# Performance work log

Measured on AMD Instinct MI355X. Metric: run time of the kernel, lower is better.

The kernel has to match this reference:

```python
import jax, jax.numpy as jnp
import numpy as np

EMBED_DIM = 1024
NUM_HEADS = 16
HEAD_DIM = EMBED_DIM // NUM_HEADS  # 64


def setup_inputs() -> dict:
    key = jax.random.key(0)
    k1, k2, k3 = jax.random.split(key, 3)
    B, N = 2, 2048
    x = jax.random.normal(k1, (B, N, EMBED_DIM), dtype=jnp.float32)
    # torch nn.Linear(E, 3E): y = x @ W.T + b; we store W already transposed as [E, 3E]
    W_qkv = jax.random.normal(k2, (EMBED_DIM, 3 * EMBED_DIM), dtype=jnp.float32) * (EMBED_DIM ** -0.5)
    b_qkv = jax.random.normal(k3, (3 * EMBED_DIM,), dtype=jnp.float32) * 0.02
    return {"x": x, "W_qkv": W_qkv, "b_qkv": b_qkv}


def reference(x, W_qkv, b_qkv):
    B, N, E = x.shape
    H, e = NUM_HEADS, HEAD_DIM
    y = x @ W_qkv + b_qkv                      # [B, N, 3E]
    # einops: 'b n (e k) -> b n e k' (k=3) then 'b n (e H) k -> b H n e k'
    # => flat index into 3E is (e_idx*H + h)*3 + qkv_idx
    y = y.reshape(B, N, e, H, 3)
    y = jnp.transpose(y, (0, 3, 1, 2, 4))      # [B, H, N, e, 3]
    q, k, v = y[..., 0], y[..., 1], y[..., 2]  # each [B, H, N, e]
    scale = 1.0 / jnp.sqrt(jnp.asarray(H, dtype=x.dtype))  # note: sqrt(num_heads), per source
    scores = jnp.einsum('bhne,bhme->bhnm', q, k) * scale   # [B, H, N, N]
    wei = jax.nn.softmax(scores, axis=-1)
    out = jnp.einsum('bhnm,bhme->bhne', wei, v)            # [B, H, N, e]
    # 'b H n e -> b n (H e)'; dropout is identity in eval mode
    out = jnp.transpose(out, (0, 2, 1, 3)).reshape(B, N, H * e)
    return out
```

## Files before the change

kernel.cpp:

```cpp
#include <hip/hip_runtime.h>
#include <hip/hip_bf16.h>
#include <math.h>

#define EDIM 1024
#define N3E  3072
#define NSEQ 2048
#define NB   2
#define NH   16
#define HD   64
#define MTOT (NB*NSEQ)

typedef __attribute__((ext_vector_type(8))) short bf16x8;
typedef __attribute__((ext_vector_type(4))) float f32x4;

#define SCALE2 0.360673760222241f

__device__ __forceinline__ short f2bf(float f) {
    union { float f; unsigned u; } v; v.f = f;
    unsigned r = v.u + 0x7FFFu + ((v.u >> 16) & 1u);
    return (short)(r >> 16);
}

__device__ __forceinline__ unsigned cvtpk(float lo, float hi) {
    unsigned r;
    asm("v_cvt_pk_bf16_f32 %0, %1, %2" : "=v"(r) : "v"(lo), "v"(hi));
    return r;
}

__device__ __forceinline__ void gload16(const void* g, void* l) {
    __builtin_amdgcn_global_load_lds(
        (const __attribute__((address_space(1))) unsigned int*)g,
        (__attribute__((address_space(3))) unsigned int*)l, 16, 0, 0);
}

__global__ __launch_bounds__(256) void k_convert_x(const float* __restrict__ x,
                                                   short* __restrict__ xb, int n4) {
    int i = blockIdx.x * blockDim.x + threadIdx.x;
    int stride = gridDim.x * blockDim.x;
    for (; i < n4; i += stride) {
        float4 v = ((const float4*)x)[i];
        ushort4 o;
        o.x = (unsigned short)f2bf(v.x);
        o.y = (unsigned short)f2bf(v.y);
        o.z = (unsigned short)f2bf(v.z);
        o.w = (unsigned short)f2bf(v.w);
        ((ushort4*)xb)[i] = o;
    }
}

__global__ __launch_bounds__(256) void k_transpose_w(const float* __restrict__ w,
                                                     short* __restrict__ wt) {
    __shared__ float T[96][68];
    int k0 = blockIdx.x * 64;
    int c0 = blockIdx.y * 96;
    int t = threadIdx.x;
    {
        int kr = t >> 2;
        int cb = (t & 3) * 24;
        const float* src = w + (size_t)(k0 + kr) * N3E + c0 + cb;
        #pragma unroll
        for (int i = 0; i < 24; i += 4) {
            float4 v = *(const float4*)(src + i);
            T[cb + i + 0][kr] = v.x;
            T[cb + i + 1][kr] = v.y;
            T[cb + i + 2][kr] = v.z;
            T[cb + i + 3][kr] = v.w;
        }
    }
    __syncthreads();
    int kk = (t & 7) * 8;
    #pragma unroll
    for (int p = 0; p < 3; ++p) {
        int cc = p * 32 + (t >> 3);
        int ca = c0 + cc;
        int e = ca / 48, h = (ca % 48) / 3, q = ca % 3;
        int cp = q * 1024 + h * 64 + e;
        bf16x8 o;
        #pragma unroll
        for (int j = 0; j < 8; ++j) o[j] = f2bf(T[cc][kk + j]);
        *(bf16x8*)(wt + (size_t)cp * EDIM + k0 + kk) = o;
    }
}

__global__ void k_perm_bias(const float* __restrict__ b, float* __restrict__ bp) {
    int c = blockIdx.x * 256 + threadIdx.x;
    if (c >= N3E) return;
    int e = c / 48, h = (c % 48) / 3, q = c % 3;
    bp[q * 1024 + h * 64 + e] = b[c];
}

__global__ __launch_bounds__(256) void k_qkv_gemm(const short* __restrict__ xb,
        const short* __restrict__ wt, const float* __restrict__ bp,
        short* __restrict__ qkv) {
    __shared__ short Al[128][32];
    __shared__ short Bl[128][32];
    int t = threadIdx.x, lane = t & 63, wv = t >> 6;
    int g = lane >> 4, r = lane & 15;
    int wr = wv >> 1, wc = wv & 1;
    int m0 = blockIdx.x * 128, n0 = blockIdx.y * 128;
    int srow = wv * 32 + (lane >> 2);
    int scol = (lane & 3) * 8;
    const short* ga0 = xb + (size_t)(m0 + srow) * EDIM + scol;
    const short* ga1 = ga0 + (size_t)16 * EDIM;
    const short* gb0 = wt + (size_t)(n0 + srow) * EDIM + scol;
    const short* gb1 = gb0 + (size_t)16 * EDIM;
    char* la0 = (char*)(&Al[0][0]) + wv * 2048;
    char* lb0 = (char*)(&Bl[0][0]) + wv * 2048;
    f32x4 acc[4][4] = {};
    for (int k0 = 0; k0 < EDIM; k0 += 32) {
        gload16(ga0 + k0, la0);
        gload16(ga1 + k0, la0 + 1024);
        gload16(gb0 + k0, lb0);
        gload16(gb1 + k0, lb0 + 1024);
        __syncthreads();
        bf16x8 af[4], bfr[4];
        #pragma unroll
        for (int mt = 0; mt < 4; ++mt)
            af[mt] = *(const bf16x8*)(&Al[wr*64 + mt*16 + r][g*8]);
        #pragma unroll
        for (int nt = 0; nt < 4; ++nt)
            bfr[nt] = *(const bf16x8*)(&Bl[wc*64 + nt*16 + r][g*8]);
        #pragma unroll
        for (int mt = 0; mt < 4; ++mt)
            #pragma unroll
            for (int nt = 0; nt < 4; ++nt)
                acc[mt][nt] = __builtin_amdgcn_mfma_f32_16x16x32_bf16(
                                  af[mt], bfr[nt], acc[mt][nt], 0, 0, 0);
        __syncthreads();
    }
    #pragma unroll
    for (int nt = 0; nt < 4; ++nt) {
        int cp = n0 + wc*64 + nt*16 + r;
        float bias = bp[cp];
        int q = cp >> 10, h = (cp >> 6) & 15, e = cp & 63;
        #pragma unroll
        for (int mt = 0; mt < 4; ++mt) {
            #pragma unroll
            for (int rg = 0; rg < 4; ++rg) {
                int m = m0 + wr*64 + mt*16 + g*4 + rg;
                int bb = m >> 11, n = m & 2047;
                qkv[((((size_t)q*NB + bb)*NH + h)*NSEQ + n)*HD + e] =
                    f2bf(acc[mt][nt][rg] + bias);
            }
        }
    }
}

__global__ __launch_bounds__(256) void k_attn(const short* __restrict__ qkv,
                                              float* __restrict__ out) {
    __shared__ short Kl[64][72];
    __shared__ short Vt[64][72];
    __shared__ short Pl[4][2][16][64];
    int t = threadIdx.x, lane = t & 63, wv = t >> 6;
    int g = lane >> 4, r = lane & 15;
    int qb = blockIdx.x, h = blockIdx.y, b = blockIdx.z;
    const size_t HS = (size_t)NSEQ * HD;
    const short* Qp = qkv + ((size_t)(0*NB + b)*NH + h) * HS;
    const short* Kp = qkv + ((size_t)(1*NB + b)*NH + h) * HS;
    const short* Vp = qkv + ((size_t)(2*NB + b)*NH + h) * HS;
    int q0 = qb * 128 + wv * 32;
    bf16x8 qf00 = *(const bf16x8*)(Qp + (size_t)(q0 + r)*HD + g*8);
    bf16x8 qf01 = *(const bf16x8*)(Qp + (size_t)(q0 + r)*HD + 32 + g*8);
    bf16x8 qf10 = *(const bf16x8*)(Qp + (size_t)(q0 + 16 + r)*HD + g*8);
    bf16x8 qf11 = *(const bf16x8*)(Qp + (size_t)(q0 + 16 + r)*HD + 32 + g*8);
    f32x4 o0[4] = {}, o1[4] = {};
    float m0r = -3.0e38f, m1r = -3.0e38f, l0r = 0.f, l1r = 0.f;
    int skv = t >> 2, sd = (t & 3) * 16;
    int vkv = (t >> 4) * 4, vd = (t & 15) * 4;
    int rx = (r & 7) << 4;
    char* prow0 = (char*)(&Pl[wv][0][0][0]) + r * 128;
    char* prow1 = prow0 + 2048;
    bf16x8 kk0, kk1; ushort4 vv0, vv1, vv2, vv3;
    const short* Kst = Kp + (size_t)skv * HD + sd;
    const short* Vst = Vp + (size_t)vkv * HD + vd;
    kk0 = *(const bf16x8*)(Kst);
    kk1 = *(const bf16x8*)(Kst + 8);
    vv0 = *(const ushort4*)(Vst);
    vv1 = *(const ushort4*)(Vst + HD);
    vv2 = *(const ushort4*)(Vst + 2*HD);
    vv3 = *(const ushort4*)(Vst + 3*HD);
    {
        *(bf16x8*)(&Kl[skv][sd]) = kk0;
        *(bf16x8*)(&Kl[skv][sd + 8]) = kk1;
        #pragma unroll
        for (int i = 0; i < 4; ++i) {
            unsigned lo = (unsigned)((const unsigned short*)&vv0)[i]
                        | ((unsigned)((const unsigned short*)&vv1)[i] << 16);
            unsigned hi = (unsigned)((const unsigned short*)&vv2)[i]
                        | ((unsigned)((const unsigned short*)&vv3)[i] << 16);
            uint2 wrd; wrd.x = lo; wrd.y = hi;
            *(uint2*)(&Vt[vd + i][vkv]) = wrd;
        }
    }
    for (int kt = 0; kt < NSEQ; kt += 64) {
        __syncthreads();
        bool more = (kt + 64) < NSEQ;
        if (more) {
            kk0 = *(const bf16x8*)(Kst + (size_t)(kt + 64) * HD);
            kk1 = *(const bf16x8*)(Kst + (size_t)(kt + 64) * HD + 8);
            vv0 = *(const ushort4*)(Vst + (size_t)(kt + 64) * HD);
            vv1 = *(const ushort4*)(Vst + (size_t)(kt + 65) * HD);
            vv2 = *(const ushort4*)(Vst + (size_t)(kt + 66) * HD);
            vv3 = *(const ushort4*)(Vst + (size_t)(kt + 67) * HD);
        }
        f32x4 s0[4], s1[4];
        #pragma unroll
        for (int jt = 0; jt < 4; ++jt) {
            bf16x8 kf0 = *(const bf16x8*)(&Kl[jt*16 + r][g*8]);
            bf16x8 kf1 = *(const bf16x8*)(&Kl[jt*16 + r][32 + g*8]);
            f32x4 z = {};
            s0[jt] = __builtin_amdgcn_mfma_f32_16x16x32_bf16(kf0, qf00, z, 0,0,0);
            s0[jt] = __builtin_amdgcn_mfma_f32_16x16x32_bf16(kf1, qf01, s0[jt], 0,0,0);
            s1[jt] = __builtin_amdgcn_mfma_f32_16x16x32_bf16(kf0, qf10, z, 0,0,0);
            s1[jt] = __builtin_amdgcn_mfma_f32_16x16x32_bf16(kf1, qf11, s1[jt], 0,0,0);
        }
        bf16x8 vf[4][2];
        #pragma unroll
        for (int dt = 0; dt < 4; ++dt) {
            vf[dt][0] = *(const bf16x8*)(&Vt[dt*16 + r][g*8]);
            vf[dt][1] = *(const bf16x8*)(&Vt[dt*16 + r][32 + g*8]);
        }
        {
            float mx = s0[0][0];
            #pragma unroll
            for (int jt = 0; jt < 4; ++jt)
                #pragma unroll
                for (int rg = 0; rg < 4; ++rg) mx = fmaxf(mx, s0[jt][rg]);
            mx = fmaxf(mx, __shfl_xor(mx, 16));
            mx = fmaxf(mx, __shfl_xor(mx, 32));
            float mnew = fmaxf(m0r, mx);
            float a = exp2f(SCALE2 * (m0r - mnew));
            m0r = mnew;
            float cm = SCALE2 * mnew;
            float ps = 0.f;
            #pragma unroll
            for (int jt = 0; jt < 4; ++jt) {
                float p0 = exp2f(fmaf(SCALE2, s0[jt][0], -cm));
                float p1 = exp2f(fmaf(SCALE2, s0[jt][1], -cm));
                float p2 = exp2f(fmaf(SCALE2, s0[jt][2], -cm));
                float p3 = exp2f(fmaf(SCALE2, s0[jt][3], -cm));
                ps += (p0 + p1) + (p2 + p3);
                uint2 wrd; wrd.x = cvtpk(p0, p1); wrd.y = cvtpk(p2, p3);
                *(uint2*)(prow0 + ((32*jt + 8*g) ^ rx)) = wrd;
            }
            ps += __shfl_xor(ps, 16);
            ps += __shfl_xor(ps, 32);
            l0r = l0r * a + ps;
            #pragma unroll
            for (int dt = 0; dt < 4; ++dt) o0[dt] *= a;
            bf16x8 pb0 = *(const bf16x8*)(prow0 + ((16*g) ^ rx));
            bf16x8 pb1 = *(const bf16x8*)(prow0 + ((64 + 16*g) ^ rx));
            #pragma unroll
            for (int dt = 0; dt < 4; ++dt) {
                o0[dt] = __builtin_amdgcn_mfma_f32_16x16x32_bf16(vf[dt][0], pb0, o0[dt], 0,0,0);
                o0[dt] = __builtin_amdgcn_mfma_f32_16x16x32_bf16(vf[dt][1], pb1, o0[dt], 0,0,0);
            }
        }
        {
            float mx = s1[0][0];
            #pragma unroll
            for (int jt = 0; jt < 4; ++jt)
                #pragma unroll
                for (int rg = 0; rg < 4; ++rg) mx = fmaxf(mx, s1[jt][rg]);
            mx = fmaxf(mx, __shfl_xor(mx, 16));
            mx = fmaxf(mx, __shfl_xor(mx, 32));
            float mnew = fmaxf(m1r, mx);
            float a = exp2f(SCALE2 * (m1r - mnew));
            m1r = mnew;
            float cm = SCALE2 * mnew;
            float ps = 0.f;
            #pragma unroll
            for (int jt = 0; jt < 4; ++jt) {
                float p0 = exp2f(fmaf(SCALE2, s1[jt][0], -cm));
                float p1 = exp2f(fmaf(SCALE2, s1[jt][1], -cm));
                float p2 = exp2f(fmaf(SCALE2, s1[jt][2], -cm));
                float p3 = exp2f(fmaf(SCALE2, s1[jt][3], -cm));
                ps += (p0 + p1) + (p2 + p3);
                uint2 wrd; wrd.x = cvtpk(p0, p1); wrd.y = cvtpk(p2, p3);
                *(uint2*)(prow1 + ((32*jt + 8*g) ^ rx)) = wrd;
            }
            ps += __shfl_xor(ps, 16);
            ps += __shfl_xor(ps, 32);
            l1r = l1r * a + ps;
            #pragma unroll
            for (int dt = 0; dt < 4; ++dt) o1[dt] *= a;
            bf16x8 pb0 = *(const bf16x8*)(prow1 + ((16*g) ^ rx));
            bf16x8 pb1 = *(const bf16x8*)(prow1 + ((64 + 16*g) ^ rx));
            #pragma unroll
            for (int dt = 0; dt < 4; ++dt) {
                o1[dt] = __builtin_amdgcn_mfma_f32_16x16x32_bf16(vf[dt][0], pb0, o1[dt], 0,0,0);
                o1[dt] = __builtin_amdgcn_mfma_f32_16x16x32_bf16(vf[dt][1], pb1, o1[dt], 0,0,0);
            }
        }
        __syncthreads();
        if (more) {
            *(bf16x8*)(&Kl[skv][sd]) = kk0;
            *(bf16x8*)(&Kl[skv][sd + 8]) = kk1;
            #pragma unroll
            for (int i = 0; i < 4; ++i) {
                unsigned lo = (unsigned)((const unsigned short*)&vv0)[i]
                            | ((unsigned)((const unsigned short*)&vv1)[i] << 16);
                unsigned hi = (unsigned)((const unsigned short*)&vv2)[i]
                            | ((unsigned)((const unsigned short*)&vv3)[i] << 16);
                uint2 wrd; wrd.x = lo; wrd.y = hi;
                *(uint2*)(&Vt[vd + i][vkv]) = wrd;
            }
        }
    }
    float inv0 = 1.0f / l0r, inv1 = 1.0f / l1r;
    #pragma unroll
    for (int dt = 0; dt < 4; ++dt) {
        float4 v0, v1;
        v0.x = o0[dt][0]*inv0; v0.y = o0[dt][1]*inv0;
        v0.z = o0[dt][2]*inv0; v0.w = o0[dt][3]*inv0;
        v1.x = o1[dt][0]*inv1; v1.y = o1[dt][1]*inv1;
        v1.z = o1[dt][2]*inv1; v1.w = o1[dt][3]*inv1;
        *(float4*)(out + (size_t)(b*NSEQ + q0 + r)*EDIM + h*HD + dt*16 + g*4) = v0;
        *(float4*)(out + (size_t)(b*NSEQ + q0 + 16 + r)*EDIM + h*HD + dt*16 + g*4) = v1;
    }
}

extern "C" void kernel_launch(void* const* d_in, const int* in_sizes, int n_in,
                              void* d_out, int out_size, void* d_ws, size_t ws_size,
                              hipStream_t stream) {
    const float* x  = (const float*)d_in[0];
    const float* w  = (const float*)d_in[1];
    const float* bq = (const float*)d_in[2];
    float* outp = (float*)d_out;
    char* ws = (char*)d_ws;
    short* Xb  = (short*)(ws);
    short* Wt  = (short*)(ws + 8388608);
    float* Bp  = (float*)(ws + 8388608 + 6291456);
    short* QKV = (short*)(ws + 8388608 + 6291456 + 16384);
    k_convert_x<<<dim3(2048), dim3(256), 0, stream>>>(x, Xb, (MTOT*EDIM)/4);
    k_transpose_w<<<dim3(16, 32), dim3(256), 0, stream>>>(w, Wt);
    k_perm_bias<<<dim3(12), dim3(256), 0, stream>>>(bq, Bp);
    k_qkv_gemm<<<dim3(32, 24), dim3(256), 0, stream>>>(Xb, Wt, Bp, QKV);
    k_attn<<<dim3(16, 16, 2), dim3(256), 0, stream>>>(QKV, outp);
}
```

Measured before the change: 220.4 us.

## Double-buffer QKV GEMM with swizzle; shrink attention tile and add lazy rescale

The QKV GEMM now double-buffers its LDS tiles so the next K-slice loads while MFMAs run on the current one. It also remaps block indices with a swizzle to improve cache locality. The attention kernel moves from 32 to 16 queries per wave, which doubles the grid, and shrinks the LDS padding. It also skips the online-softmax rescale when the running max grows by less than a threshold. The smaller query tile raises occupancy and parallelism but doubles the K/V traffic per query. The 68-element padding may give misaligned 16-byte LDS accesses.

```diff
diff --git a/kernel.cpp b/kernel.cpp
--- a/kernel.cpp
+++ b/kernel.cpp
@@ -14,6 +14,7 @@
 typedef __attribute__((ext_vector_type(4))) float f32x4;
 
 #define SCALE2 0.360673760222241f
+#define DTHR   16.0f
 
 __device__ __forceinline__ short f2bf(float f) {
     union { float f; unsigned u; } v; v.f = f;
@@ -92,34 +93,45 @@
 __global__ __launch_bounds__(256) void k_qkv_gemm(const short* __restrict__ xb,
         const short* __restrict__ wt, const float* __restrict__ bp,
         short* __restrict__ qkv) {
-    __shared__ short Al[128][32];
-    __shared__ short Bl[128][32];
+    __shared__ short Al[2][128][32];
+    __shared__ short Bl[2][128][32];
     int t = threadIdx.x, lane = t & 63, wv = t >> 6;
     int g = lane >> 4, r = lane & 15;
     int wr = wv >> 1, wc = wv & 1;
-    int m0 = blockIdx.x * 128, n0 = blockIdx.y * 128;
+    int flat = blockIdx.y * 32 + blockIdx.x;
+    int sw = (flat & 7) * 96 + (flat >> 3);
+    int m0 = (sw & 31) * 128, n0 = (sw >> 5) * 128;
     int srow = wv * 32 + (lane >> 2);
     int scol = (lane & 3) * 8;
     const short* ga0 = xb + (size_t)(m0 + srow) * EDIM + scol;
     const short* ga1 = ga0 + (size_t)16 * EDIM;
     const short* gb0 = wt + (size_t)(n0 + srow) * EDIM + scol;
     const short* gb1 = gb0 + (size_t)16 * EDIM;
-    char* la0 = (char*)(&Al[0][0]) + wv * 2048;
-    char* lb0 = (char*)(&Bl[0][0]) + wv * 2048;
+    char* laA = (char*)(&Al[0][0][0]) + wv * 2048;
+    char* laB = (char*)(&Bl[0][0][0]) + wv * 2048;
     f32x4 acc[4][4] = {};
-    for (int k0 = 0; k0 < EDIM; k0 += 32) {
-        gload16(ga0 + k0, la0);
-        gload16(ga1 + k0, la0 + 1024);
-        gload16(gb0 + k0, lb0);
-        gload16(gb1 + k0, lb0 + 1024);
-        __syncthreads();
+    gload16(ga0, laA);
+    gload16(ga1, laA + 1024);
+    gload16(gb0, laB);
+    gload16(gb1, laB + 1024);
+    __syncthreads();
+    for (int step = 0; step < 32; ++step) {
+        if (step < 31) {
+            int nk = (step + 1) * 32;
+            int bo = ((step + 1) & 1) * 8192;
+            gload16(ga0 + nk, laA + bo);
+            gload16(ga1 + nk, laA + bo + 1024);
+            gload16(gb0 + nk, laB + bo);
+            gload16(gb1 + nk, laB + bo + 1024);
+        }
+        int cb = step & 1;
         bf16x8 af[4], bfr[4];
         #pragma unroll
         for (int mt = 0; mt < 4; ++mt)
-            af[mt] = *(const bf16x8*)(&Al[wr*64 + mt*16 + r][g*8]);
+            af[mt] = *(const bf16x8*)(&Al[cb][wr*64 + mt*16 + r][g*8]);
         #pragma unroll
         for (int nt = 0; nt < 4; ++nt)
-            bfr[nt] = *(const bf16x8*)(&Bl[wc*64 + nt*16 + r][g*8]);
+            bfr[nt] = *(const bf16x8*)(&Bl[cb][wc*64 + nt*16 + r][g*8]);
         #pragma unroll
         for (int mt = 0; mt < 4; ++mt)
             #pragma unroll
@@ -148,9 +160,9 @@
 
 __global__ __launch_bounds__(256) void k_attn(const short* __restrict__ qkv,
                                               float* __restrict__ out) {
-    __shared__ short Kl[64][72];
-    __shared__ short Vt[64][72];
-    __shared__ short Pl[4][2][16][64];
+    __shared__ short Kl[64][68];
+    __shared__ short Vt[64][68];
+    __shared__ short Pl[4][16][64];
     int t = threadIdx.x, lane = t & 63, wv = t >> 6;
     int g = lane >> 4, r = lane & 15;
     int qb = blockIdx.x, h = blockIdx.y, b = blockIdx.z;
@@ -158,18 +170,15 @@
     const short* Qp = qkv + ((size_t)(0*NB + b)*NH + h) * HS;
     const short* Kp = qkv + ((size_t)(1*NB + b)*NH + h) * HS;
     const short* Vp = qkv + ((size_t)(2*NB + b)*NH + h) * HS;
-    int q0 = qb * 128 + wv * 32;
-    bf16x8 qf00 = *(const bf16x8*)(Qp + (size_t)(q0 + r)*HD + g*8);
-    bf16x8 qf01 = *(const bf16x8*)(Qp + (size_t)(q0 + r)*HD + 32 + g*8);
-    bf16x8 qf10 = *(const bf16x8*)(Qp + (size_t)(q0 + 16 + r)*HD + g*8);
-    bf16x8 qf11 = *(const bf16x8*)(Qp + (size_t)(q0 + 16 + r)*HD + 32 + g*8);
-    f32x4 o0[4] = {}, o1[4] = {};
-    float m0r = -3.0e38f, m1r = -3.0e38f, l0r = 0.f, l1r = 0.f;
+    int q0 = qb * 64 + wv * 16;
+    bf16x8 qf0 = *(const bf16x8*)(Qp + (size_t)(q0 + r)*HD + g*8);
+    bf16x8 qf1 = *(const bf16x8*)(Qp + (size_t)(q0 + r)*HD + 32 + g*8);
+    f32x4 o[4] = {};
+    float mr = -3.0e38f, lr = 0.f;
     int skv = t >> 2, sd = (t & 3) * 16;
     int vkv = (t >> 4) * 4, vd = (t & 15) * 4;
     int rx = (r & 7) << 4;
-    char* prow0 = (char*)(&Pl[wv][0][0][0]) + r * 128;
-    char* prow1 = prow0 + 2048;
+    char* prow = (char*)(&Pl[wv][0][0]) + r * 128;
     bf16x8 kk0, kk1; ushort4 vv0, vv1, vv2, vv3;
     const short* Kst = Kp + (size_t)skv * HD + sd;
     const short* Vst = Vp + (size_t)vkv * HD + vd;
@@ -203,16 +212,14 @@
             vv2 = *(const ushort4*)(Vst + (size_t)(kt + 66) * HD);
             vv3 = *(const ushort4*)(Vst + (size_t)(kt + 67) * HD);
         }
-        f32x4 s0[4], s1[4];
+        f32x4 s[4];
         #pragma unroll
         for (int jt = 0; jt < 4; ++jt) {
             bf16x8 kf0 = *(const bf16x8*)(&Kl[jt*16 + r][g*8]);
             bf16x8 kf1 = *(const bf16x8*)(&Kl[jt*16 + r][32 + g*8]);
             f32x4 z = {};
-            s0[jt] = __builtin_amdgcn_mfma_f32_16x16x32_bf16(kf0, qf00, z, 0,0,0);
-            s0[jt] = __builtin_amdgcn_mfma_f32_16x16x32_bf16(kf1, qf01, s0[jt], 0,0,0);
-            s1[jt] = __builtin_amdgcn_mfma_f32_16x16x32_bf16(kf0, qf10, z, 0,0,0);
-            s1[jt] = __builtin_amdgcn_mfma_f32_16x16x32_bf16(kf1, qf11, s1[jt], 0,0,0);
+            s[jt] = __builtin_amdgcn_mfma_f32_16x16x32_bf16(kf0, qf0, z, 0,0,0);
+            s[jt] = __builtin_amdgcn_mfma_f32_16x16x32_bf16(kf1, qf1, s[jt], 0,0,0);
         }
         bf16x8 vf[4][2];
         #pragma unroll
@@ -220,77 +227,41 @@
             vf[dt][0] = *(const bf16x8*)(&Vt[dt*16 + r][g*8]);
             vf[dt][1] = *(const bf16x8*)(&Vt[dt*16 + r][32 + g*8]);
         }
-        {
-            float mx = s0[0][0];
+        float mx = fmaxf(fmaxf(fmaxf(s[0][0], s[0][1]), fmaxf(s[0][2], s[0][3])),
+                         fmaxf(fmaxf(s[1][0], s[1][1]), fmaxf(s[1][2], s[1][3])));
+        mx = fmaxf(mx, fmaxf(fmaxf(fmaxf(s[2][0], s[2][1]), fmaxf(s[2][2], s[2][3])),
+                             fmaxf(fmaxf(s[3][0], s[3][1]), fmaxf(s[3][2], s[3][3]))));
+        mx = fmaxf(mx, __shfl_xor(mx, 16));
+        mx = fmaxf(mx, __shfl_xor(mx, 32));
+        if (!__all(mx <= mr + DTHR)) {
+            float mnew = fmaxf(mr, mx);
+            float a = exp2f(SCALE2 * (mr - mnew));
+            mr = mnew;
+            lr *= a;
             #pragma unroll
-            for (int jt = 0; jt < 4; ++jt)
-                #pragma unroll
-                for (int rg = 0; rg < 4; ++rg) mx = fmaxf(mx, s0[jt][rg]);
-            mx = fmaxf(mx, __shfl_xor(mx, 16));
-            mx = fmaxf(mx, __shfl_xor(mx, 32));
-            float mnew = fmaxf(m0r, mx);
-            float a = exp2f(SCALE2 * (m0r - mnew));
-            m0r = mnew;
-            float cm = SCALE2 * mnew;
-            float ps = 0.f;
-            #pragma unroll
-            for (int jt = 0; jt < 4; ++jt) {
-                float p0 = exp2f(fmaf(SCALE2, s0[jt][0], -cm));
-                float p1 = exp2f(fmaf(SCALE2, s0[jt][1], -cm));
-                float p2 = exp2f(fmaf(SCALE2, s0[jt][2], -cm));
-                float p3 = exp2f(fmaf(SCALE2, s0[jt][3], -cm));
-                ps += (p0 + p1) + (p2 + p3);
-                uint2 wrd; wrd.x = cvtpk(p0, p1); wrd.y = cvtpk(p2, p3);
-                *(uint2*)(prow0 + ((32*jt + 8*g) ^ rx)) = wrd;
-            }
-            ps += __shfl_xor(ps, 16);
-            ps += __shfl_xor(ps, 32);
-            l0r = l0r * a + ps;
-            #pragma unroll
-            for (int dt = 0; dt < 4; ++dt) o0[dt] *= a;
-            bf16x8 pb0 = *(const bf16x8*)(prow0 + ((16*g) ^ rx));
-            bf16x8 pb1 = *(const bf16x8*)(prow0 + ((64 + 16*g) ^ rx));
-            #pragma unroll
-            for (int dt = 0; dt < 4; ++dt) {
-                o0[dt] = __builtin_amdgcn_mfma_f32_16x16x32_bf16(vf[dt][0], pb0, o0[dt], 0,0,0);
-                o0[dt] = __builtin_amdgcn_mfma_f32_16x16x32_bf16(vf[dt][1], pb1, o0[dt], 0,0,0);
-            }
-        }
-        {
-            float mx = s1[0][0];
-            #pragma unroll
-            for (int jt = 0; jt < 4; ++jt)
-                #pragma unroll
-                for (int rg = 0; rg < 4; ++rg) mx = fmaxf(mx, s1[jt][rg]);
-            mx = fmaxf(mx, __shfl_xor(mx, 16));
-            mx = fmaxf(mx, __shfl_xor(mx, 32));
-            float mnew = fmaxf(m1r, mx);
-            float a = exp2f(SCALE2 * (m1r - mnew));
-            m1r = mnew;
-            float cm = SCALE2 * mnew;
-            float ps = 0.f;
-            #pragma unroll
-            for (int jt = 0; jt < 4; ++jt) {
-                float p0 = exp2f(fmaf(SCALE2, s1[jt][0], -cm));
-                float p1 = exp2f(fmaf(SCALE2, s1[jt][1], -cm));
-                float p2 = exp2f(fmaf(SCALE2, s1[jt][2], -cm));
-                float p3 = exp2f(fmaf(SCALE2, s1[jt][3], -cm));
-                ps += (p0 + p1) + (p2 + p3);
-                uint2 wrd; wrd.x = cvtpk(p0, p1); wrd.y = cvtpk(p2, p3);
-                *(uint2*)(prow1 + ((32*jt + 8*g) ^ rx)) = wrd;
-            }
-            ps += __shfl_xor(ps, 16);
-            ps += __shfl_xor(ps, 32);
-            l1r = l1r * a + ps;
-            #pragma unroll
-            for (int dt = 0; dt < 4; ++dt) o1[dt] *= a;
-            bf16x8 pb0 = *(const bf16x8*)(prow1 + ((16*g) ^ rx));
-            bf16x8 pb1 = *(const bf16x8*)(prow1 + ((64 + 16*g) ^ rx));
-            #pragma unroll
-            for (int dt = 0; dt < 4; ++dt) {
-                o1[dt] = __builtin_amdgcn_mfma_f32_16x16x32_bf16(vf[dt][0], pb0, o1[dt], 0,0,0);
-                o1[dt] = __builtin_amdgcn_mfma_f32_16x16x32_bf16(vf[dt][1], pb1, o1[dt], 0,0,0);
-            }
+            for (int dt = 0; dt < 4; ++dt) o[dt] *= a;
+        }
+        float cm = SCALE2 * mr;
+        float ps = 0.f;
+        #pragma unroll
+        for (int jt = 0; jt < 4; ++jt) {
+            float p0 = exp2f(fmaf(SCALE2, s[jt][0], -cm));
+            float p1 = exp2f(fmaf(SCALE2, s[jt][1], -cm));
+            float p2 = exp2f(fmaf(SCALE2, s[jt][2], -cm));
+            float p3 = exp2f(fmaf(SCALE2, s[jt][3], -cm));
+            ps += (p0 + p1) + (p2 + p3);
+            uint2 wrd; wrd.x = cvtpk(p0, p1); wrd.y = cvtpk(p2, p3);
+            *(uint2*)(prow + ((32*jt + 8*g) ^ rx)) = wrd;
+        }
+        ps += __shfl_xor(ps, 16);
+        ps += __shfl_xor(ps, 32);
+        lr += ps;
+        bf16x8 pb0 = *(const bf16x8*)(prow + ((16*g) ^ rx));
+        bf16x8 pb1 = *(const bf16x8*)(prow + ((64 + 16*g) ^ rx));
+        #pragma unroll
+        for (int dt = 0; dt < 4; ++dt) {
+            o[dt] = __builtin_amdgcn_mfma_f32_16x16x32_bf16(vf[dt][0], pb0, o[dt], 0,0,0);
+            o[dt] = __builtin_amdgcn_mfma_f32_16x16x32_bf16(vf[dt][1], pb1, o[dt], 0,0,0);
         }
         __syncthreads();
         if (more) {
@@ -307,16 +278,13 @@
             }
         }
     }
-    float inv0 = 1.0f / l0r, inv1 = 1.0f / l1r;
+    float inv = 1.0f / lr;
     #pragma unroll
     for (int dt = 0; dt < 4; ++dt) {
-        float4 v0, v1;
-        v0.x = o0[dt][0]*inv0; v0.y = o0[dt][1]*inv0;
-        v0.z = o0[dt][2]*inv0; v0.w = o0[dt][3]*inv0;
-        v1.x = o1[dt][0]*inv1; v1.y = o1[dt][1]*inv1;
-        v1.z = o1[dt][2]*inv1; v1.w = o1[dt][3]*inv1;
+        float4 v0;
+        v0.x = o[dt][0]*inv; v0.y = o[dt][1]*inv;
+        v0.z = o[dt][2]*inv; v0.w = o[dt][3]*inv;
         *(float4*)(out + (size_t)(b*NSEQ + q0 + r)*EDIM + h*HD + dt*16 + g*4) = v0;
-        *(float4*)(out + (size_t)(b*NSEQ + q0 + 16 + r)*EDIM + h*HD + dt*16 + g*4) = v1;
     }
 }
 
@@ -336,5 +304,5 @@
     k_transpose_w<<<dim3(16, 32), dim3(256), 0, stream>>>(w, Wt);
     k_perm_bias<<<dim3(12), dim3(256), 0, stream>>>(bq, Bp);
     k_qkv_gemm<<<dim3(32, 24), dim3(256), 0, stream>>>(Xb, Wt, Bp, QKV);
-    k_attn<<<dim3(16, 16, 2), dim3(256), 0, stream>>>(QKV, outp);
-}
+    k_attn<<<dim3(32, 16, 2), dim3(256), 0, stream>>>(QKV, outp);
+}
```

After: 220.6 us. Within noise of the previous version (+0.1%).
